# Kernel tuning notes

Hardware: AMD Instinct MI355X
Metric: run time of the kernel (lower is better)

The kernel has to match this reference:

```python
import jax, jax.numpy as jnp
import numpy as np

NUM_HEADS = 32
NUM_KV_GROUPS = 8


def _rope(x, cos, sin):
    # x: [B, H, S, hd]; cos/sin: [S_max, hd]
    S, hd = x.shape[2], x.shape[3]
    x1, x2 = x[..., : hd // 2], x[..., hd // 2 :]
    rotated = jnp.concatenate((-x2, x1), axis=-1)
    c = cos[:S][None, None]
    s = sin[:S][None, None]
    return (x * c + rotated * s).astype(x.dtype)


def setup_inputs() -> dict:
    key = jax.random.key(0)
    ks = jax.random.split(key, 8)
    B, S, D = 2, 2048, 2048
    H, G = NUM_HEADS, NUM_KV_GROUPS
    hd = D // H
    scale = 1.0 / np.sqrt(D)
    return {
        "inputs": jax.random.normal(ks[0], (B, S, D), jnp.float32),
        "mask": jnp.zeros((S, S), jnp.bool_),  # note: original masked_fill is not in-place -> mask unused
        "cos": jax.random.uniform(ks[1], (S, hd), jnp.float32),
        "sin": jax.random.uniform(ks[2], (S, hd), jnp.float32),
        "Wq": jax.random.normal(ks[3], (D, H * hd), jnp.float32) * scale,
        "Wk": jax.random.normal(ks[4], (D, G * hd), jnp.float32) * scale,
        "Wv": jax.random.normal(ks[5], (D, G * hd), jnp.float32) * scale,
        "Wo": jax.random.normal(ks[6], (H * hd, H * hd), jnp.float32) * scale,
    }


def reference(inputs, mask, cos, sin, Wq, Wk, Wv, Wo):
    B, S, D = inputs.shape
    H, G = NUM_HEADS, NUM_KV_GROUPS
    hd = Wq.shape[1] // H
    group_size = H // G

    q = (inputs @ Wq).reshape(B, S, H, hd).transpose(0, 2, 1, 3)  # [B,H,S,hd]
    k = (inputs @ Wk).reshape(B, S, G, hd).transpose(0, 2, 1, 3)  # [B,G,S,hd]
    v = (inputs @ Wv).reshape(B, S, G, hd).transpose(0, 2, 1, 3)

    q = _rope(q, cos, sin)
    k = _rope(k, cos, sin)

    k = jnp.repeat(k, group_size, axis=1)  # [B,H,S,hd]
    v = jnp.repeat(v, group_size, axis=1)

    scores = jnp.einsum("bhqd,bhkd->bhqk", q, k)
    # NOTE: original uses non-inplace masked_fill whose result is discarded,
    # so faithfully NO mask is applied.
    attn = jax.nn.softmax(scores / jnp.sqrt(jnp.float32(hd)).astype(scores.dtype), axis=-1)
    ctx = jnp.einsum("bhqk,bhkd->bhqd", attn, v)
    ctx = ctx.transpose(0, 2, 1, 3).reshape(B, S, H * hd)
    return ctx @ Wo
```

## Files before the change

### kernel.cpp

```cpp
#include <hip/hip_runtime.h>
#include <stdint.h>

typedef __attribute__((ext_vector_type(8))) short short8;
typedef __attribute__((ext_vector_type(4))) short short4v;
typedef __attribute__((ext_vector_type(4))) float float4v;
typedef __attribute__((ext_vector_type(2))) unsigned uint2v;

__device__ __forceinline__ float bf2f(short s) {
  union { unsigned u; float f; } x;
  x.u = ((unsigned)(unsigned short)s) << 16;
  return x.f;
}
__device__ __forceinline__ short f2bf(float f) {
  union { float f; unsigned u; } x;
  x.f = f;
  unsigned r = x.u + 0x7fffu + ((x.u >> 16) & 1u);
  return (short)(r >> 16);
}
__device__ __forceinline__ float fexp2(float x) {
#if __has_builtin(__builtin_amdgcn_exp2f)
  return __builtin_amdgcn_exp2f(x);
#else
  float r;
  asm("v_exp_f32 %0, %1" : "=v"(r) : "v"(x));
  return r;
#endif
}
__device__ __forceinline__ void glds16(const void* g, void* l) {
  __builtin_amdgcn_global_load_lds(
      (const __attribute__((address_space(1))) void*)g,
      (__attribute__((address_space(3))) void*)l, 16, 0, 0);
}

__global__ __launch_bounds__(256) void f32_to_bf16(const float* __restrict__ s,
                                                   short* __restrict__ d) {
  const long i = ((long)blockIdx.x * 256 + threadIdx.x) * 8;
  const float4v a = *(const float4v*)&s[i];
  const float4v b = *(const float4v*)&s[i + 4];
  short8 v;
#pragma unroll
  for (int e = 0; e < 4; ++e) { v[e] = f2bf(a[e]); v[e + 4] = f2bf(b[e]); }
  *(short8*)&d[i] = v;
}

__device__ __forceinline__ void transpose_tile(
    const float* __restrict__ src, short* __restrict__ dst, int R, int C,
    int r0, int c0) {
  __shared__ short t[64 * 72];
  const int tid = threadIdx.x;
#pragma unroll
  for (int r = 0; r < 2; ++r) {
    int c = r * 256 + tid;
    int row = c >> 3, col8 = (c & 7) * 8;
    const float4v a = *(const float4v*)&src[(long)(r0 + row) * C + c0 + col8];
    const float4v b = *(const float4v*)&src[(long)(r0 + row) * C + c0 + col8 + 4];
    short8 v;
#pragma unroll
    for (int e = 0; e < 4; ++e) { v[e] = f2bf(a[e]); v[e + 4] = f2bf(b[e]); }
    *(short8*)&t[row * 72 + col8] = v;
  }
  __syncthreads();
#pragma unroll
  for (int r = 0; r < 2; ++r) {
    int c = r * 256 + tid;
    int orow = c >> 3, ocol8 = (c & 7) * 8;
    short8 w;
#pragma unroll
    for (int e = 0; e < 8; ++e) w[e] = t[(ocol8 + e) * 72 + orow];
    *(short8*)&dst[(long)(c0 + orow) * R + r0 + ocol8] = w;
  }
}

__global__ __launch_bounds__(256) void transpose_f2b(
    const float* __restrict__ src, short* __restrict__ dst, int R, int C) {
  transpose_tile(src, dst, R, C, blockIdx.y * 64, blockIdx.x * 64);
}

__global__ __launch_bounds__(256) void wtrans3(
    const float* __restrict__ Wq, const float* __restrict__ Wk,
    const float* __restrict__ Wv, short* __restrict__ WT) {
  const int z = blockIdx.z;
  const float* src = z == 0 ? Wq : (z == 1 ? Wk : Wv);
  const int C = z == 0 ? 2048 : 512;
  if (blockIdx.x * 64 >= C) return;
  short* dst = WT + (z == 0 ? 0 : (z == 1 ? 2048 * 2048 : 2560 * 2048));
  transpose_tile(src, dst, 2048, C, blockIdx.y * 64, blockIdx.x * 64);
}

__global__ __launch_bounds__(256) void vtrans(const short* __restrict__ Y,
                                              short* __restrict__ Vt,
                                              int ld, int col0) {
  const int bg = blockIdx.y;
  const int b = bg >> 3, gk = bg & 7;
  const int s0 = blockIdx.x * 64;
  __shared__ short t[64 * 72];
  const int tid = threadIdx.x;
#pragma unroll
  for (int r = 0; r < 2; ++r) {
    int c = r * 256 + tid;
    int row = c >> 3, col8 = (c & 7) * 8;
    short8 v = *(const short8*)&Y[(long)(b * 2048 + s0 + row) * ld + col0 + gk * 64 + col8];
    *(short8*)&t[row * 72 + col8] = v;
  }
  __syncthreads();
#pragma unroll
  for (int r = 0; r < 2; ++r) {
    int c = r * 256 + tid;
    int d = c >> 3, s8 = (c & 7) * 8;
    short8 w;
#pragma unroll
    for (int e = 0; e < 8; ++e) w[e] = t[(s8 + e) * 72 + d];
    *(short8*)&Vt[((long)bg * 64 + d) * 2048 + s0 + s8] = w;
  }
}

__global__ __launch_bounds__(256) void rope_kernel(
    const short* __restrict__ Y, const float* __restrict__ cosp,
    const float* __restrict__ sinp, short* __restrict__ out,
    int NH, int lgNH, int ld, int col0, float scale) {
  const long tid = (long)blockIdx.x * 256 + threadIdx.x;
  const int d = (int)(tid & 31);
  const long t1 = tid >> 5;
  const int h = (int)(t1 & (NH - 1));
  const long t2 = t1 >> lgNH;
  const int s = (int)(t2 & 2047);
  const int b = (int)(t2 >> 11);
  const long ib = (long)(b * 2048 + s) * ld + col0 + h * 64 + d;
  const float x1 = bf2f(Y[ib]);
  const float x2 = bf2f(Y[ib + 32]);
  const float c1 = cosp[s * 64 + d];
  const float c2 = cosp[s * 64 + d + 32];
  const float s1 = sinp[s * 64 + d];
  const float s2 = sinp[s * 64 + d + 32];
  const long ob = ((long)(b * NH + h) * 2048 + s) * 64 + d;
  out[ob] = f2bf((x1 * c1 - x2 * s1) * scale);
  out[ob + 32] = f2bf((x2 * c2 + x1 * s2) * scale);
}

template <typename OutT>
__global__ __launch_bounds__(256) void gemm_bt(
    const short* __restrict__ A, const short* __restrict__ BT,
    OutT* __restrict__ C, int M, int N, int K) {
  __shared__ short As[128 * 32];
  __shared__ short Bs[128 * 32];
  const int tid = threadIdx.x;
  const int wave = tid >> 6, lane = tid & 63;
  const int g = lane >> 4, lr = lane & 15;
  const int m0 = blockIdx.y * 128, n0 = blockIdx.x * 128;
  const int wr = wave >> 1, wc = wave & 1;

  float4v acc[4][4];
#pragma unroll
  for (int i = 0; i < 4; ++i)
#pragma unroll
    for (int j = 0; j < 4; ++j) acc[i][j] = (float4v)0.f;

  for (int kt = 0; kt < K; kt += 32) {
#pragma unroll
    for (int r = 0; r < 2; ++r) {
      const int cb = r * 256 + wave * 64;
      const int c = cb + lane;
      const int row = c >> 2, kc = c & 3;
      glds16(A + (long)(m0 + row) * K + kt + kc * 8, As + cb * 8);
      glds16(BT + (long)(n0 + row) * K + kt + kc * 8, Bs + cb * 8);
    }
    __syncthreads();
    short8 af[4], bfr[4];
#pragma unroll
    for (int i = 0; i < 4; ++i)
      af[i] = *(const short8*)&As[(wr * 64 + i * 16 + lr) * 32 + g * 8];
#pragma unroll
    for (int j = 0; j < 4; ++j)
      bfr[j] = *(const short8*)&Bs[(wc * 64 + j * 16 + lr) * 32 + g * 8];
#pragma unroll
    for (int i = 0; i < 4; ++i)
#pragma unroll
      for (int j = 0; j < 4; ++j)
        acc[i][j] = __builtin_amdgcn_mfma_f32_16x16x32_bf16(af[i], bfr[j], acc[i][j], 0, 0, 0);
    __syncthreads();
  }

#pragma unroll
  for (int i = 0; i < 4; ++i)
#pragma unroll
    for (int j = 0; j < 4; ++j)
#pragma unroll
      for (int t = 0; t < 4; ++t) {
        const int r = m0 + wr * 64 + i * 16 + g * 4 + t;
        const int cc = n0 + wc * 64 + j * 16 + lr;
        float v = acc[i][j][t];
        if constexpr (sizeof(OutT) == 2)
          C[(long)r * N + cc] = f2bf(v);
        else
          C[(long)r * N + cc] = v;
      }
}

__global__ __launch_bounds__(512, 2) void attn_kernel(
    const short* __restrict__ Qr, const short* __restrict__ Kr,
    const short* __restrict__ Vt, short* __restrict__ Ctx) {
  constexpr int S = 2048;
  const int bh = blockIdx.y;
  const int b = bh >> 5, h = bh & 31;
  const int gk = h >> 2;
  const int q0 = blockIdx.x << 7;
  const int tid = threadIdx.x;
  const int w = tid >> 6, lane = tid & 63;
  const int g = lane >> 4, lr = lane & 15;
  const int b8 = lr & 7;
  const int qrow = w * 16 + lr;

  __shared__ short Ks[128 * 64];
  __shared__ short Vs[64 * 128];
  __shared__ short Ps[128 * 128];

  const short* Qb = Qr + (long)(b * 32 + h) * S * 64;
  const short* KbIt = Kr + (long)(b * 8 + gk) * S * 64;
  const short* VbIt = Vt + (long)(b * 8 + gk) * 64 * S;

  const int ko0 = lr * 64 + ((0 + g) ^ b8) * 8;
  const int ko1 = lr * 64 + ((4 + g) ^ b8) * 8;
  const int jv0 = g ^ b8;
  const int vo0 = lr * 128 + jv0 * 8;
  const int vo1 = lr * 128 + (jv0 ^ 4) * 8;
  int pr[4], pw[8];
#pragma unroll
  for (int ks = 0; ks < 4; ++ks) pr[ks] = qrow * 128 + ((4 * ks + g) ^ b8) * 8;
#pragma unroll
  for (int i = 0; i < 8; ++i)
    pw[i] = qrow * 128 + ((2 * i + (g >> 1)) ^ b8) * 8 + (g & 1) * 4;

  long koff[2], voff[2];
#pragma unroll
  for (int r = 0; r < 2; ++r) {
    const int c = r * 512 + w * 64 + lane;
    const int kv = c >> 3, slot = c & 7;
    koff[r] = (long)kv * 64 + (slot ^ (kv & 7)) * 8;
    const int dd = c >> 4, s16 = c & 15;
    voff[r] = (long)dd * S + ((s16 & 8) | ((s16 & 7) ^ (dd & 7))) * 8;
  }

  short8 qf[2];
  qf[0] = *(const short8*)&Qb[(long)(q0 + qrow) * 64 + g * 8];
  qf[1] = *(const short8*)&Qb[(long)(q0 + qrow) * 64 + 32 + g * 8];

  const short8 ones = (short8)(short)0x3F80;
  float4v lacc = (float4v)0.f;
  float4v oacc[4];
#pragma unroll
  for (int di = 0; di < 4; ++di) oacc[di] = (float4v)0.f;

  for (int it = 0; it < 16; ++it) {
#pragma unroll
    for (int r = 0; r < 2; ++r) {
      const int cb = r * 512 + w * 64;
      glds16(KbIt + koff[r], Ks + cb * 8);
      glds16(VbIt + voff[r], Vs + cb * 8);
    }
    __syncthreads();

    float4v sacc[8];
#pragma unroll
    for (int i = 0; i < 8; ++i) sacc[i] = (float4v)0.f;
#pragma unroll
    for (int i = 0; i < 8; ++i) {
      const short8 a0 = *(const short8*)&Ks[ko0 + i * 1024];
      sacc[i] = __builtin_amdgcn_mfma_f32_16x16x32_bf16(a0, qf[0], sacc[i], 0, 0, 0);
    }
#pragma unroll
    for (int i = 0; i < 8; ++i) {
      const short8 a1 = *(const short8*)&Ks[ko1 + i * 1024];
      sacc[i] = __builtin_amdgcn_mfma_f32_16x16x32_bf16(a1, qf[1], sacc[i], 0, 0, 0);
    }

#pragma unroll
    for (int i = 0; i < 8; ++i) {
      union { float f; unsigned u; } a0, a1, a2, a3;
      a0.f = fexp2(sacc[i][0]);
      a1.f = fexp2(sacc[i][1]);
      a2.f = fexp2(sacc[i][2]);
      a3.f = fexp2(sacc[i][3]);
      const unsigned d0 = __builtin_amdgcn_perm(a1.u + 0x8000u, a0.u + 0x8000u, 0x07060302u);
      const unsigned d1 = __builtin_amdgcn_perm(a3.u + 0x8000u, a2.u + 0x8000u, 0x07060302u);
      *(uint2v*)&Ps[pw[i]] = (uint2v){d0, d1};
    }

#pragma unroll
    for (int ks = 0; ks < 4; ++ks) {
      const short8 pf = *(const short8*)&Ps[pr[ks]];
      const int vbase = (ks & 1) ? vo1 : vo0;
      lacc = __builtin_amdgcn_mfma_f32_16x16x32_bf16(ones, pf, lacc, 0, 0, 0);
#pragma unroll
      for (int di = 0; di < 4; ++di) {
        const short8 vf = *(const short8*)&Vs[vbase + di * 2048 + (ks >> 1) * 64];
        oacc[di] = __builtin_amdgcn_mfma_f32_16x16x32_bf16(vf, pf, oacc[di], 0, 0, 0);
      }
    }
    __syncthreads();
    KbIt += 128 * 64;
    VbIt += 128;
  }

  const float inv = 1.f / lacc[0];

  const int q = q0 + qrow;
#pragma unroll
  for (int di = 0; di < 4; ++di) {
    short4v o;
#pragma unroll
    for (int t = 0; t < 4; ++t) o[t] = f2bf(oacc[di][t] * inv);
    *(short4v*)&Ctx[(long)(b * S + q) * 2048 + h * 64 + di * 16 + g * 4] = o;
  }
}

extern "C" void kernel_launch(void* const* d_in, const int* in_sizes, int n_in,
                              void* d_out, int out_size, void* d_ws, size_t ws_size,
                              hipStream_t stream) {
  (void)in_sizes; (void)n_in; (void)out_size; (void)ws_size;
  const float* X    = (const float*)d_in[0];
  const float* cosp = (const float*)d_in[2];
  const float* sinp = (const float*)d_in[3];
  const float* Wq   = (const float*)d_in[4];
  const float* Wk   = (const float*)d_in[5];
  const float* Wv   = (const float*)d_in[6];
  const float* Wo   = (const float*)d_in[7];
  float* out = (float*)d_out;
  char* ws = (char*)d_ws;

  short* Xb = (short*)(ws + 0);
  short* WT = (short*)(ws + 16777216);
  short* Y  = (short*)(ws + 29360128);
  short* Qr = (short*)(ws + 54525952);
  short* Kr = (short*)(ws + 71303168);
  short* Vt = (short*)(ws + 75497472);

  f32_to_bf16<<<4096, 256, 0, stream>>>(X, Xb);
  wtrans3<<<dim3(32, 32, 3), 256, 0, stream>>>(Wq, Wk, Wv, WT);

  gemm_bt<short><<<dim3(24, 32), 256, 0, stream>>>(Xb, WT, Y, 4096, 3072, 2048);

  transpose_f2b<<<dim3(32, 32), 256, 0, stream>>>(Wo, WT, 2048, 2048);

  rope_kernel<<<16384, 256, 0, stream>>>(Y, cosp, sinp, Qr, 32, 5, 3072, 0, 0.18033688011112043f);
  rope_kernel<<<4096, 256, 0, stream>>>(Y, cosp, sinp, Kr, 8, 3, 3072, 2048, 1.0f);
  vtrans<<<dim3(32, 16), 256, 0, stream>>>(Y, Vt, 3072, 2560);

  attn_kernel<<<dim3(16, 64), 512, 0, stream>>>(Qr, Kr, Vt, Y);

  gemm_bt<float><<<dim3(16, 32), 256, 0, stream>>>(Y, WT, out, 4096, 2048, 2048);
}
```

Baseline: 374.7 us.

## Replace GEMM with 256x256 double-buffered, swizzled, interleaved MFMA pipeline

Replaces the 128x128, single-buffered GEMM used for the QKV and output projections with a 256x256 tile kernel on 512 threads. It uses K-step 64, two LDS buffers prefetched two iterations ahead, XOR-swizzled LDS columns, and quarter-wise interleaving of LDS reads, global-to-LDS loads and MFMA blocks under sched barriers and priority hints. The aim is to raise arithmetic intensity and hide global load latency behind matrix math. In exchange, far fewer blocks are launched (192 and 128 on a large-CU GPU), so occupancy and wave quantization may suffer. Register pressure also rises with 128 accumulators per thread.

```diff
diff --git a/kernel.cpp b/kernel.cpp
--- a/kernel.cpp
+++ b/kernel.cpp
@@ -30,6 +30,11 @@
   __builtin_amdgcn_global_load_lds(
       (const __attribute__((address_space(1))) void*)g,
       (__attribute__((address_space(3))) void*)l, 16, 0, 0);
+}
+__device__ __forceinline__ void sbar() {
+  __builtin_amdgcn_sched_barrier(0);
+  __builtin_amdgcn_s_barrier();
+  __builtin_amdgcn_sched_barrier(0);
 }
 
 __global__ __launch_bounds__(256) void f32_to_bf16(const float* __restrict__ s,
@@ -138,62 +143,123 @@
 }
 
 template <typename OutT>
-__global__ __launch_bounds__(256) void gemm_bt(
+__global__ __launch_bounds__(512, 2) void gemm256(
     const short* __restrict__ A, const short* __restrict__ BT,
     OutT* __restrict__ C, int M, int N, int K) {
-  __shared__ short As[128 * 32];
-  __shared__ short Bs[128 * 32];
+  (void)M;
+  __shared__ short As[2][16384];
+  __shared__ short Bs[2][16384];
   const int tid = threadIdx.x;
-  const int wave = tid >> 6, lane = tid & 63;
+  const int w = tid >> 6, lane = tid & 63;
   const int g = lane >> 4, lr = lane & 15;
-  const int m0 = blockIdx.y * 128, n0 = blockIdx.x * 128;
-  const int wr = wave >> 1, wc = wave & 1;
-
-  float4v acc[4][4];
-#pragma unroll
-  for (int i = 0; i < 4; ++i)
+  const int wm = w >> 2, wn = w & 3;
+  const int m0 = blockIdx.y << 8, n0 = blockIdx.x << 8;
+
+  const int r0 = tid >> 3;
+  const int scol = ((tid & 7) << 3) ^ (((r0 >> 2) & 1) << 4);
+  const long aoff = (long)(m0 + r0) * K + scol;
+  const long boff = (long)(n0 + r0) * K + scol;
+
+  const int swz = ((lr >> 2) & 1) << 4;
+  const int acol0 = (g << 3) ^ swz;
+  const int acol1 = (32 + (g << 3)) ^ swz;
+  const int abase = (wm * 128 + lr) * 64;
+  const int bbase = (wn * 64 + lr) * 64;
+
+  float4v acc[8][4];
+#pragma unroll
+  for (int i = 0; i < 8; ++i)
 #pragma unroll
     for (int j = 0; j < 4; ++j) acc[i][j] = (float4v)0.f;
 
-  for (int kt = 0; kt < K; kt += 32) {
-#pragma unroll
-    for (int r = 0; r < 2; ++r) {
-      const int cb = r * 256 + wave * 64;
-      const int c = cb + lane;
-      const int row = c >> 2, kc = c & 3;
-      glds16(A + (long)(m0 + row) * K + kt + kc * 8, As + cb * 8);
-      glds16(BT + (long)(n0 + row) * K + kt + kc * 8, Bs + cb * 8);
-    }
-    __syncthreads();
-    short8 af[4], bfr[4];
-#pragma unroll
-    for (int i = 0; i < 4; ++i)
-      af[i] = *(const short8*)&As[(wr * 64 + i * 16 + lr) * 32 + g * 8];
+#define STAGE_A(l, buf, kg)                                          \
+  glds16(A + aoff + (long)(l) * 64 * K + (kg),                       \
+         &As[(buf)][(l) * 4096 + w * 512])
+#define STAGE_B(l, buf, kg)                                          \
+  glds16(BT + boff + (long)(l) * 64 * K + (kg),                      \
+         &Bs[(buf)][(l) * 4096 + w * 512])
+
+  const int NT = K >> 6;
+#pragma unroll
+  for (int l = 0; l < 4; ++l) { STAGE_A(l, 0, 0); STAGE_B(l, 0, 0); }
+#pragma unroll
+  for (int l = 0; l < 4; ++l) { STAGE_A(l, 1, 64); STAGE_B(l, 1, 64); }
+  asm volatile("s_waitcnt vmcnt(8)" ::: "memory");
+  sbar();
+
+  short8 aR[4][2], bR0[2][2], bR1[2][2];
+
+#define LDA(MH, ASB)                                                       \
+  _Pragma("unroll") for (int i = 0; i < 4; ++i) {                          \
+    aR[i][0] = *(const short8*)&ASB[abase + ((MH)*4 + i) * 1024 + acol0];  \
+    aR[i][1] = *(const short8*)&ASB[abase + ((MH)*4 + i) * 1024 + acol1];  \
+  }
+#define LDB(NH, BSB, BR)                                                   \
+  _Pragma("unroll") for (int j = 0; j < 2; ++j) {                          \
+    BR[j][0] = *(const short8*)&BSB[bbase + ((NH)*2 + j) * 1024 + acol0];  \
+    BR[j][1] = *(const short8*)&BSB[bbase + ((NH)*2 + j) * 1024 + acol1];  \
+  }
+#define MMA_Q(MH, NH, BR)                                                  \
+  __builtin_amdgcn_s_setprio(1);                                           \
+  _Pragma("unroll") for (int kk = 0; kk < 2; ++kk)                         \
+  _Pragma("unroll") for (int i = 0; i < 4; ++i)                            \
+  _Pragma("unroll") for (int j = 0; j < 2; ++j)                            \
+    acc[(MH)*4 + i][(NH)*2 + j] = __builtin_amdgcn_mfma_f32_16x16x32_bf16( \
+        aR[i][kk], BR[j][kk], acc[(MH)*4 + i][(NH)*2 + j], 0, 0, 0);       \
+  __builtin_amdgcn_s_setprio(0);
+
+  for (int t = 0; t < NT; ++t) {
+    const short* const Asb = As[t & 1];
+    const short* const Bsb = Bs[t & 1];
+    const long kg = (long)(t + 2) << 6;
+    const bool pre = (t + 2) < NT;
+
+    LDA(0, Asb);
+    LDB(0, Bsb, bR0);
+    sbar();
+    MMA_Q(0, 0, bR0);
+    sbar();
+    LDB(1, Bsb, bR1);
+    if (pre) { STAGE_A(0, t & 1, kg); STAGE_A(2, t & 1, kg); }
+    sbar();
+    MMA_Q(0, 1, bR1);
+    sbar();
+    LDA(1, Asb);
+    if (pre) {
+      STAGE_B(0, t & 1, kg); STAGE_B(1, t & 1, kg);
+      STAGE_B(2, t & 1, kg); STAGE_B(3, t & 1, kg);
+    }
+    sbar();
+    MMA_Q(1, 1, bR1);
+    sbar();
+    if (pre) { STAGE_A(1, t & 1, kg); STAGE_A(3, t & 1, kg); }
+    sbar();
+    MMA_Q(1, 0, bR0);
+    __builtin_amdgcn_sched_barrier(0);
+    if (pre) { asm volatile("s_waitcnt vmcnt(8)" ::: "memory"); }
+    else     { asm volatile("s_waitcnt vmcnt(0)" ::: "memory"); }
+    sbar();
+  }
+
+#pragma unroll
+  for (int i = 0; i < 8; ++i)
 #pragma unroll
     for (int j = 0; j < 4; ++j)
-      bfr[j] = *(const short8*)&Bs[(wc * 64 + j * 16 + lr) * 32 + g * 8];
-#pragma unroll
-    for (int i = 0; i < 4; ++i)
-#pragma unroll
-      for (int j = 0; j < 4; ++j)
-        acc[i][j] = __builtin_amdgcn_mfma_f32_16x16x32_bf16(af[i], bfr[j], acc[i][j], 0, 0, 0);
-    __syncthreads();
-  }
-
-#pragma unroll
-  for (int i = 0; i < 4; ++i)
-#pragma unroll
-    for (int j = 0; j < 4; ++j)
-#pragma unroll
-      for (int t = 0; t < 4; ++t) {
-        const int r = m0 + wr * 64 + i * 16 + g * 4 + t;
-        const int cc = n0 + wc * 64 + j * 16 + lr;
-        float v = acc[i][j][t];
+#pragma unroll
+      for (int t4 = 0; t4 < 4; ++t4) {
+        const int r = m0 + wm * 128 + i * 16 + g * 4 + t4;
+        const int cc = n0 + wn * 64 + j * 16 + lr;
+        const float v = acc[i][j][t4];
         if constexpr (sizeof(OutT) == 2)
           C[(long)r * N + cc] = f2bf(v);
         else
           C[(long)r * N + cc] = v;
       }
+#undef STAGE_A
+#undef STAGE_B
+#undef LDA
+#undef LDB
+#undef MMA_Q
 }
 
 __global__ __launch_bounds__(512, 2) void attn_kernel(
@@ -337,7 +403,7 @@
   f32_to_bf16<<<4096, 256, 0, stream>>>(X, Xb);
   wtrans3<<<dim3(32, 32, 3), 256, 0, stream>>>(Wq, Wk, Wv, WT);
 
-  gemm_bt<short><<<dim3(24, 32), 256, 0, stream>>>(Xb, WT, Y, 4096, 3072, 2048);
+  gemm256<short><<<dim3(12, 16), 512, 0, stream>>>(Xb, WT, Y, 4096, 3072, 2048);
 
   transpose_f2b<<<dim3(32, 32), 256, 0, stream>>>(Wo, WT, 2048, 2048);
 
@@ -347,5 +413,5 @@
 
   attn_kernel<<<dim3(16, 64), 512, 0, stream>>>(Qr, Kr, Vt, Y);
 
-  gemm_bt<float><<<dim3(16, 32), 256, 0, stream>>>(Y, WT, out, 4096, 2048, 2048);
-}
+  gemm256<float><<<dim3(8, 16), 512, 0, stream>>>(Y, WT, out, 4096, 2048, 2048);
+}
```

New measurement: 386.4 us. +3.1%, slower.
